# Performance work log

Hardware: AMD Instinct MI355X
Metric: run time of the kernel (lower is better)

The kernel has to match this reference:

```python
import jax, jax.numpy as jnp
import numpy as np

NUM_HEADS = 12


def setup_inputs() -> dict:
    key = jax.random.key(0)
    k1, k2, k3 = jax.random.split(key, 3)
    B, T, N, D = 8, 8, 196, 768
    x = jax.random.normal(k1, (B, T * N, D), dtype=jnp.float32)
    w_qkv = jax.random.normal(k2, (D, 3 * D), dtype=jnp.float32) * 0.02
    w_proj = jax.random.normal(k3, (D, D), dtype=jnp.float32) * 0.02
    b_proj = jnp.zeros((D,), dtype=jnp.float32)
    return {"x": x, "T": T, "N": N, "w_qkv": w_qkv, "w_proj": w_proj, "b_proj": b_proj}


def reference(x, T, N, w_qkv, w_proj, b_proj):
    B, TN, D = x.shape
    H = NUM_HEADS
    hd = D // H
    scale = hd ** -0.5
    # qkv projection: (B, TN, 3, H, hd)
    qkv = (x @ w_qkv).reshape(B, TN, 3, H, hd)
    # -> (3, B, H, T, N, hd)
    qkv = jnp.transpose(qkv, (2, 0, 3, 1, 4)).reshape(3, B, H, T, N, hd)
    q, k, v = qkv[0], qkv[1], qkv[2]

    # Temporal branch: mean-pool over spatial axis N (keepdim -> length-1 attn axis)
    q_t = q.mean(axis=3, keepdims=True)            # (B,H,T,1,hd)
    k_t = k.mean(axis=3, keepdims=True)            # (B,H,T,1,hd)
    v_t = v.mean(axis=3, keepdims=True)            # (B,H,T,1,hd)
    attn_t = jnp.einsum('bhtqd,bhtkd->bhtqk', q_t, k_t) * scale  # (B,H,T,1,1)
    attn_t = jax.nn.softmax(attn_t, axis=-1)
    x_t = jnp.einsum('bhtqk,bhtkd->bhtqd', attn_t, v_t)[:, :, :, 0]  # (B,H,T,hd)

    # Spatial branch: full attention within each frame
    attn_s = jnp.einsum('bhtnd,bhtmd->bhtnm', q, k) * scale  # (B,H,T,N,N)
    attn_s = jax.nn.softmax(attn_s, axis=-1)
    x_s = jnp.einsum('bhtnm,bhtmd->bhtnd', attn_s, v)        # (B,H,T,N,hd)

    # Combine: broadcast temporal result over spatial positions, add
    out = x_s + x_t[:, :, :, None, :]                        # (B,H,T,N,hd)
    out = out.reshape(B, H, T * N, hd)
    out = jnp.transpose(out, (0, 2, 1, 3)).reshape(B * T * N, D)
    return out @ w_proj + b_proj
```

## Files before the change

### kernel.cpp

```cpp
#include <hip/hip_runtime.h>
#include <math.h>

#define BB 8
#define TT 8
#define NN 196
#define DD 768
#define HH 12
#define HD 64
#define TN (TT * NN)
#define MM (BB * TN)
#define D3 (3 * DD)

typedef _Float16 f16;
typedef _Float16 f16x8 __attribute__((ext_vector_type(8)));
typedef _Float16 f16x4 __attribute__((ext_vector_type(4)));
typedef float f32x4 __attribute__((ext_vector_type(4)));
typedef unsigned int u32;

#define GLDS16(gp, lp)                                                        \
  __builtin_amdgcn_global_load_lds(                                           \
      (const __attribute__((address_space(1))) u32*)(gp),                     \
      (__attribute__((address_space(3))) u32*)(lp), 16, 0, 0)

#define MFMA16(a, b, c) __builtin_amdgcn_mfma_f32_16x16x32_f16(a, b, c, 0, 0, 0)

__global__ __launch_bounds__(256) void gemm_f16nt(
    const f16* __restrict__ A, const f16* __restrict__ Bt,
    float* __restrict__ C32, f16* __restrict__ C16, int K, int Ncol,
    const float* __restrict__ bias, int mode) {
  __shared__ f16 As[128 * 64];
  __shared__ f16 Bs[128 * 64];

  const int tid = threadIdx.x;
  const int lane = tid & 63;
  const int wave = tid >> 6;
  const int wy = wave >> 1, wx = wave & 1;
  const int bm = blockIdx.y * 128;
  const int bn = blockIdx.x * 128;

  const f16* aP[4];
  const f16* bP[4];
#pragma unroll
  for (int it = 0; it < 4; it++) {
    int ci = tid + it * 256;
    int r = ci >> 3;
    int c = (ci & 7) ^ (r & 7);
    aP[it] = A + (size_t)(bm + r) * K + c * 8;
    bP[it] = Bt + (size_t)(bn + r) * K + c * 8;
  }

  f32x4 acc[4][4];
#pragma unroll
  for (int i = 0; i < 4; i++)
#pragma unroll
    for (int j = 0; j < 4; j++) acc[i][j] = (f32x4)0.0f;

  const int fr = lane & 15;
  const int q = lane >> 4;
  const int sw = fr & 7;

  for (int kt = 0; kt < K; kt += 64) {
#pragma unroll
    for (int it = 0; it < 4; it++) {
      GLDS16(aP[it] + kt, &As[(tid + it * 256) * 8]);
      GLDS16(bP[it] + kt, &Bs[(tid + it * 256) * 8]);
    }
    __syncthreads();

#pragma unroll
    for (int kk = 0; kk < 2; kk++) {
      const int lc = ((kk * 4 + q) ^ sw) * 8;
      f16x8 af[4], bf[4];
#pragma unroll
      for (int mi = 0; mi < 4; mi++)
        af[mi] = *(const f16x8*)&As[(wy * 64 + mi * 16 + fr) * 64 + lc];
#pragma unroll
      for (int ni = 0; ni < 4; ni++)
        bf[ni] = *(const f16x8*)&Bs[(wx * 64 + ni * 16 + fr) * 64 + lc];

#pragma unroll
      for (int mi = 0; mi < 4; mi++)
#pragma unroll
        for (int ni = 0; ni < 4; ni++)
          acc[mi][ni] = MFMA16(af[mi], bf[ni], acc[mi][ni]);
    }
    __syncthreads();
  }

  if (mode == 0) {
#pragma unroll
    for (int mi = 0; mi < 4; mi++) {
      const int row0 = bm + wy * 64 + mi * 16 + (lane >> 4) * 4;
#pragma unroll
      for (int ni = 0; ni < 4; ni++) {
        const int col = bn + wx * 64 + ni * 16 + (lane & 15);
        float bv = (bias != nullptr) ? bias[col] : 0.0f;
#pragma unroll
        for (int r = 0; r < 4; r++)
          C32[(size_t)(row0 + r) * Ncol + col] = acc[mi][ni][r] + bv;
      }
    }
  } else {
#pragma unroll
    for (int mi = 0; mi < 4; mi++) {
      const int row0 = bm + wy * 64 + mi * 16 + (lane >> 4) * 4;
#pragma unroll
      for (int r = 0; r < 4; r++) {
        const int token = row0 + r;
        const int f = token / NN;
        const int n = token - f * NN;
        f16* fb = C16 + ((size_t)f * (HH * 3) * NN) * 64 + n * 64;
#pragma unroll
        for (int ni = 0; ni < 4; ni++) {
          const int col = bn + wx * 64 + ni * 16 + (lane & 15);
          const int qt = col / DD;
          const int rem = col - qt * DD;
          const int hh = rem >> 6;
          const int d = rem & 63;
          fb[(size_t)(hh * 3 + qt) * NN * 64 + d] = (f16)acc[mi][ni][r];
        }
      }
    }
  }
}

__global__ __launch_bounds__(256) void conv_f32_to_f16(
    const float* __restrict__ in, f16* __restrict__ out, int n4) {
  int i = blockIdx.x * blockDim.x + threadIdx.x;
  const int stride = gridDim.x * blockDim.x;
  for (; i < n4; i += stride) {
    float4 f = ((const float4*)in)[i];
    f16x4 h;
    h[0] = (f16)f.x;
    h[1] = (f16)f.y;
    h[2] = (f16)f.z;
    h[3] = (f16)f.w;
    ((f16x4*)out)[i] = h;
  }
}

__global__ __launch_bounds__(256) void transpose_f32_to_f16(
    const float* __restrict__ W, f16* __restrict__ Wt, int K, int Ncol) {
  __shared__ float tileS[32][33];
  const int k0 = blockIdx.y * 32, n0 = blockIdx.x * 32;
  const int tx = threadIdx.x & 31, ty = threadIdx.x >> 5;
#pragma unroll
  for (int i = 0; i < 4; i++)
    tileS[ty + i * 8][tx] = W[(size_t)(k0 + ty + i * 8) * Ncol + n0 + tx];
  __syncthreads();
#pragma unroll
  for (int i = 0; i < 4; i++)
    Wt[(size_t)(n0 + ty + i * 8) * K + k0 + tx] = (f16)tileS[tx][ty + i * 8];
}

#define VSTR 232

__global__ __launch_bounds__(512, 4) void attn_mfma(
    const f16* __restrict__ qkv, f16* __restrict__ out) {
  __shared__ f16 KS[196 * 64];
  __shared__ f16 VS[64 * VSTR];
  __shared__ __align__(16) f16 PS[8 * 16 * 40];
  __shared__ float vmean[64];
  float* red = (float*)PS;

  const int bi = blockIdx.x;
  const int t = bi % TT;
  const int h = (bi / TT) % HH;
  const int b = bi / (TT * HH);
  const int frame = b * TT + t;
  const int tok0 = frame * NN;

  const f16* Qb = qkv + (size_t)(frame * HH + h) * 3 * NN * 64;
  const f16* Kb = Qb + NN * 64;
  const f16* Vb = Qb + 2 * NN * 64;

  const int tid = threadIdx.x;
  const int lane = tid & 63;
  const int wave = tid >> 6;
  const int m = lane & 15;
  const int q = lane >> 4;

#pragma unroll
  for (int it = 0; it < 3; it++) {
    int chunk = tid + it * 512;
    int row = chunk >> 3, pc = chunk & 7;
    int c = pc ^ (row & 7);
    GLDS16(Kb + row * 64 + c * 8, &KS[chunk * 8]);
  }
  if (tid < 32) {
    int chunk = 1536 + tid;
    int row = chunk >> 3, pc = chunk & 7;
    int c = pc ^ (row & 7);
    *(f16x8*)&KS[chunk * 8] = *(const f16x8*)(Kb + row * 64 + c * 8);
  }

  for (int idx = tid; idx < 64 * 9; idx += 512) {
    int d = idx / 9, c = idx % 9;
    *(f16x4*)&VS[d * VSTR + 196 + c * 4] = (f16x4){0, 0, 0, 0};
  }

  const int vd = tid & 63;
  const int kb = tid >> 6;
  float vpart = 0.0f;
  if (kb < 7) {
#pragma unroll
    for (int it = 0; it < 7; it++) {
      int k0 = kb * 28 + it * 4;
      f16x4 pk;
#pragma unroll
      for (int j = 0; j < 4; j++) {
        f16 v = Vb[(k0 + j) * 64 + vd];
        pk[j] = v;
        vpart += (float)v;
      }
      *(f16x4*)&VS[vd * VSTR + k0] = pk;
    }
  }
  red[tid] = vpart;
  __syncthreads();
  if (tid < 64) {
    float s = 0.0f;
#pragma unroll
    for (int g = 0; g < 8; g++) s += red[tid + 64 * g];
    vmean[tid] = s * (1.0f / (float)NN);
  }
  __syncthreads();

  f16* PSw = &PS[wave * 640];

  for (int qt = wave; qt < 13; qt += 8) {
    const int q0 = qt * 16;
    int qrow = q0 + m;
    if (qrow > NN - 1) qrow = NN - 1;
    const f16* qbase = Qb + qrow * 64;
    f16x8 aq0 = *(const f16x8*)(qbase + q * 8);
    f16x8 aq1 = *(const f16x8*)(qbase + 32 + q * 8);

    f32x4 o0 = (f32x4)0.0f, o1 = (f32x4)0.0f, o2 = (f32x4)0.0f,
          o3 = (f32x4)0.0f;
    float l[4] = {0.0f, 0.0f, 0.0f, 0.0f};

    for (int ch = 0; ch < 7; ch++) {
      const int keyA = ch * 32 + m;
      const int keyB = keyA + 16;
      const int kA = keyA > 195 ? 195 : keyA;
      const int kB = keyB > 195 ? 195 : keyB;
      const int swA = kA & 7, swB = kB & 7;
      f16x8 b00 = *(const f16x8*)&KS[kA * 64 + ((q ^ swA) * 8)];
      f16x8 b01 = *(const f16x8*)&KS[kA * 64 + (((q + 4) ^ swA) * 8)];
      f16x8 b10 = *(const f16x8*)&KS[kB * 64 + ((q ^ swB) * 8)];
      f16x8 b11 = *(const f16x8*)&KS[kB * 64 + (((q + 4) ^ swB) * 8)];
      f32x4 z = (f32x4)0.0f;
      f32x4 s0 = MFMA16(aq0, b00, z);
      s0 = MFMA16(aq1, b01, s0);
      f32x4 s1 = MFMA16(aq0, b10, z);
      s1 = MFMA16(aq1, b11, s1);

      const bool v0 = keyA < NN;
      const bool v1 = keyB < NN;
#pragma unroll
      for (int r = 0; r < 4; r++) {
        float p0 = v0 ? __expf(s0[r] * 0.125f) : 0.0f;
        float p1 = v1 ? __expf(s1[r] * 0.125f) : 0.0f;
        l[r] += p0 + p1;
        PSw[(q * 4 + r) * 40 + m] = (f16)p0;
        PSw[(q * 4 + r) * 40 + 16 + m] = (f16)p1;
      }
      f16x8 pa = *(const f16x8*)&PSw[m * 40 + q * 8];
      f16x8 bv0 = *(const f16x8*)&VS[(0 * 16 + m) * VSTR + ch * 32 + q * 8];
      f16x8 bv1 = *(const f16x8*)&VS[(1 * 16 + m) * VSTR + ch * 32 + q * 8];
      f16x8 bv2 = *(const f16x8*)&VS[(2 * 16 + m) * VSTR + ch * 32 + q * 8];
      f16x8 bv3 = *(const f16x8*)&VS[(3 * 16 + m) * VSTR + ch * 32 + q * 8];
      o0 = MFMA16(pa, bv0, o0);
      o1 = MFMA16(pa, bv1, o1);
      o2 = MFMA16(pa, bv2, o2);
      o3 = MFMA16(pa, bv3, o3);
    }

#pragma unroll
    for (int r = 0; r < 4; r++) {
      float s = l[r];
      s += __shfl_xor(s, 1);
      s += __shfl_xor(s, 2);
      s += __shfl_xor(s, 4);
      s += __shfl_xor(s, 8);
      l[r] = 1.0f / s;
    }

#pragma unroll
    for (int r = 0; r < 4; r++) {
      const int query = q0 + q * 4 + r;
      if (query < NN) {
        f16* orow = out + (size_t)(tok0 + query) * DD + h * HD;
        orow[m] = (f16)(o0[r] * l[r] + vmean[m]);
        orow[16 + m] = (f16)(o1[r] * l[r] + vmean[16 + m]);
        orow[32 + m] = (f16)(o2[r] * l[r] + vmean[32 + m]);
        orow[48 + m] = (f16)(o3[r] * l[r] + vmean[48 + m]);
      }
    }
  }
}

extern "C" void kernel_launch(void* const* d_in, const int* in_sizes, int n_in,
                              void* d_out, int out_size, void* d_ws,
                              size_t ws_size, hipStream_t stream) {
  (void)in_sizes;
  (void)n_in;
  (void)out_size;
  (void)ws_size;
  const float* x      = (const float*)d_in[0];
  const float* w_qkv  = (const float*)d_in[3];
  const float* w_proj = (const float*)d_in[4];
  const float* b_proj = (const float*)d_in[5];
  float* out = (float*)d_out;

  char* ws = (char*)d_ws;
  f16* qkvh = (f16*)ws;
  f16* xh = (f16*)(ws + (size_t)MM * D3 * 2);
  f16* wqkvT = xh + (size_t)MM * DD;
  f16* wprojT = wqkvT + (size_t)D3 * DD;

  conv_f32_to_f16<<<2048, 256, 0, stream>>>(x, xh, MM * DD / 4);
  transpose_f32_to_f16<<<dim3(D3 / 32, DD / 32), 256, 0, stream>>>(w_qkv,
                                                                   wqkvT, DD, D3);
  transpose_f32_to_f16<<<dim3(DD / 32, DD / 32), 256, 0, stream>>>(w_proj,
                                                                   wprojT, DD, DD);
  gemm_f16nt<<<dim3(D3 / 128, MM / 128), 256, 0, stream>>>(
      xh, wqkvT, nullptr, qkvh, DD, D3, nullptr, 1);
  attn_mfma<<<BB * HH * TT, 512, 0, stream>>>(qkvh, xh);
  gemm_f16nt<<<dim3(DD / 128, MM / 128), 256, 0, stream>>>(
      xh, wprojT, out, nullptr, DD, DD, b_proj, 0);
}
```

Measured before the change: 234.1 us.

## Remap GEMM blocks per XCD and read attention keys directly from global

Both GEMMs now launch a flat grid and remap block IDs so that consecutive blocks on the same XCD share an M row-band and iterate over N tiles. The aim is better L2 reuse of the A rows; surplus blocks exit early. The attention kernel no longer stages K into LDS. Each wave loads K rows straight from global memory, and the occupancy hint is raised from 4 to 6 blocks. This trades repeated global/L1 reads of K for less LDS use and more resident waves. Keys past the end of the frame read into the V region, and those values are masked out.

```diff
diff --git a/kernel.cpp b/kernel.cpp
--- a/kernel.cpp
+++ b/kernel.cpp
@@ -27,16 +27,23 @@
 __global__ __launch_bounds__(256) void gemm_f16nt(
     const f16* __restrict__ A, const f16* __restrict__ Bt,
     float* __restrict__ C32, f16* __restrict__ C16, int K, int Ncol,
-    const float* __restrict__ bias, int mode) {
+    const float* __restrict__ bias, int mode, int mTiles, int nTiles) {
   __shared__ f16 As[128 * 64];
   __shared__ f16 Bs[128 * 64];
+
+  const int flat = blockIdx.x;
+  const int xcd = flat & 7;
+  const int j = flat >> 3;
+  const int mb = xcd + 8 * (j / nTiles);
+  const int nb = j % nTiles;
+  if (mb >= mTiles) return;
+  const int bm = mb * 128;
+  const int bn = nb * 128;
 
   const int tid = threadIdx.x;
   const int lane = tid & 63;
   const int wave = tid >> 6;
   const int wy = wave >> 1, wx = wave & 1;
-  const int bm = blockIdx.y * 128;
-  const int bn = blockIdx.x * 128;
 
   const f16* aP[4];
   const f16* bP[4];
@@ -53,7 +60,7 @@
 #pragma unroll
   for (int i = 0; i < 4; i++)
 #pragma unroll
-    for (int j = 0; j < 4; j++) acc[i][j] = (f32x4)0.0f;
+    for (int j2 = 0; j2 < 4; j2++) acc[i][j2] = (f32x4)0.0f;
 
   const int fr = lane & 15;
   const int q = lane >> 4;
@@ -155,9 +162,8 @@
 
 #define VSTR 232
 
-__global__ __launch_bounds__(512, 4) void attn_mfma(
+__global__ __launch_bounds__(512, 6) void attn_mfma(
     const f16* __restrict__ qkv, f16* __restrict__ out) {
-  __shared__ f16 KS[196 * 64];
   __shared__ f16 VS[64 * VSTR];
   __shared__ __align__(16) f16 PS[8 * 16 * 40];
   __shared__ float vmean[64];
@@ -179,20 +185,6 @@
   const int wave = tid >> 6;
   const int m = lane & 15;
   const int q = lane >> 4;
-
-#pragma unroll
-  for (int it = 0; it < 3; it++) {
-    int chunk = tid + it * 512;
-    int row = chunk >> 3, pc = chunk & 7;
-    int c = pc ^ (row & 7);
-    GLDS16(Kb + row * 64 + c * 8, &KS[chunk * 8]);
-  }
-  if (tid < 32) {
-    int chunk = 1536 + tid;
-    int row = chunk >> 3, pc = chunk & 7;
-    int c = pc ^ (row & 7);
-    *(f16x8*)&KS[chunk * 8] = *(const f16x8*)(Kb + row * 64 + c * 8);
-  }
 
   for (int idx = tid; idx < 64 * 9; idx += 512) {
     int d = idx / 9, c = idx % 9;
@@ -243,13 +235,12 @@
     for (int ch = 0; ch < 7; ch++) {
       const int keyA = ch * 32 + m;
       const int keyB = keyA + 16;
-      const int kA = keyA > 195 ? 195 : keyA;
-      const int kB = keyB > 195 ? 195 : keyB;
-      const int swA = kA & 7, swB = kB & 7;
-      f16x8 b00 = *(const f16x8*)&KS[kA * 64 + ((q ^ swA) * 8)];
-      f16x8 b01 = *(const f16x8*)&KS[kA * 64 + (((q + 4) ^ swA) * 8)];
-      f16x8 b10 = *(const f16x8*)&KS[kB * 64 + ((q ^ swB) * 8)];
-      f16x8 b11 = *(const f16x8*)&KS[kB * 64 + (((q + 4) ^ swB) * 8)];
+      const f16* kra = Kb + keyA * 64;
+      const f16* krb = Kb + keyB * 64;
+      f16x8 b00 = *(const f16x8*)(kra + q * 8);
+      f16x8 b01 = *(const f16x8*)(kra + 32 + q * 8);
+      f16x8 b10 = *(const f16x8*)(krb + q * 8);
+      f16x8 b11 = *(const f16x8*)(krb + 32 + q * 8);
       f32x4 z = (f32x4)0.0f;
       f32x4 s0 = MFMA16(aq0, b00, z);
       s0 = MFMA16(aq1, b01, s0);
@@ -325,9 +316,9 @@
                                                                    wqkvT, DD, D3);
   transpose_f32_to_f16<<<dim3(DD / 32, DD / 32), 256, 0, stream>>>(w_proj,
                                                                    wprojT, DD, DD);
-  gemm_f16nt<<<dim3(D3 / 128, MM / 128), 256, 0, stream>>>(
-      xh, wqkvT, nullptr, qkvh, DD, D3, nullptr, 1);
+  gemm_f16nt<<<8 * 13 * 18, 256, 0, stream>>>(
+      xh, wqkvT, nullptr, qkvh, DD, D3, nullptr, 1, 98, 18);
   attn_mfma<<<BB * HH * TT, 512, 0, stream>>>(qkvh, xh);
-  gemm_f16nt<<<dim3(DD / 128, MM / 128), 256, 0, stream>>>(
-      xh, wprojT, out, nullptr, DD, DD, b_proj, 0);
-}
+  gemm_f16nt<<<8 * 13 * 6, 256, 0, stream>>>(
+      xh, wprojT, out, nullptr, DD, DD, b_proj, 0, 98, 6);
+}
```

After: 290.3 us. 1.24x slower.
